# Performance work log

Hardware: AMD Instinct MI355X
Metric: run time of the kernel (lower is better)

## Reference

```python
import jax, jax.numpy as jnp
import numpy as np
import math

B = 16
IMG = 224
P = 16
C_IN = 3
E = 768
H = 12
HD = E // H          # 64
D = 6                # depth
MLP = 3072
NC = 1000
GH = IMG // P        # 14
N = GH * GH + 1      # 197 tokens incl cls
LAMBDA_INIT = 0.8
EPS = 1e-5


def setup_inputs() -> dict:
    key = jax.random.key(0)
    ks = jax.random.split(key, 24)
    s = 0.02
    inp = {
        "x": jax.random.normal(ks[0], (B, C_IN, IMG, IMG), jnp.float32),
        "conv_w": jax.random.normal(ks[1], (E, C_IN, P, P), jnp.float32) * s,
        "conv_b": jnp.zeros((E,), jnp.float32),
        "cls_token": jax.random.normal(ks[2], (1, 1, E), jnp.float32) * s,
        "pos_embed": jax.random.normal(ks[3], (1, N, E), jnp.float32) * s,
        # per-layer stacked params (leading dim D)
        "Wq": jax.random.normal(ks[4], (D, E, 2 * E), jnp.float32) * s,
        "Wk": jax.random.normal(ks[5], (D, E, 2 * E), jnp.float32) * s,
        "Wv": jax.random.normal(ks[6], (D, E, 2 * E), jnp.float32) * s,
        "lq1": jax.random.normal(ks[7], (D, H, HD), jnp.float32) * 0.1,
        "lk1": jax.random.normal(ks[8], (D, H, HD), jnp.float32) * 0.1,
        "lq2": jax.random.normal(ks[9], (D, H, HD), jnp.float32) * 0.1,
        "lk2": jax.random.normal(ks[10], (D, H, HD), jnp.float32) * 0.1,
        "gn_g": jnp.ones((D, 2 * HD), jnp.float32),
        "gn_b": jnp.zeros((D, 2 * HD), jnp.float32),
        "Wo": jax.random.normal(ks[11], (D, 2 * E, E), jnp.float32) * s,
        "ln1_g": jnp.ones((D, E), jnp.float32),
        "ln1_b": jnp.zeros((D, E), jnp.float32),
        "ln2_g": jnp.ones((D, E), jnp.float32),
        "ln2_b": jnp.zeros((D, E), jnp.float32),
        "mlp_w1": jax.random.normal(ks[12], (D, E, MLP), jnp.float32) * s,
        "mlp_b1": jnp.zeros((D, MLP), jnp.float32),
        "mlp_w2": jax.random.normal(ks[13], (D, MLP, E), jnp.float32) * s,
        "mlp_b2": jnp.zeros((D, E), jnp.float32),
        "lnf_g": jnp.ones((E,), jnp.float32),
        "lnf_b": jnp.zeros((E,), jnp.float32),
        "head_w": jax.random.normal(ks[14], (E, NC), jnp.float32) * s,
        "head_b": jnp.zeros((NC,), jnp.float32),
    }
    return inp


def _ln(z, g, b):
    m = jnp.mean(z, axis=-1, keepdims=True)
    v = jnp.var(z, axis=-1, keepdims=True)
    return (z - m) * jax.lax.rsqrt(v + EPS) * g + b


def _forward(x, conv_w, conv_b, cls_token, pos_embed, Wq, Wk, Wv,
             lq1, lk1, lq2, lk2, gn_g, gn_b, Wo,
             ln1_g, ln1_b, ln2_g, ln2_b,
             mlp_w1, mlp_b1, mlp_w2, mlp_b2,
             lnf_g, lnf_b, head_w, head_b):
    Bx = x.shape[0]
    # patch embedding (conv stride=kernel == non-overlapping patch matmul)
    xp = x.reshape(Bx, C_IN, GH, P, GH, P)
    tok = jnp.einsum('bchpwq,ecpq->bhwe', xp, conv_w).reshape(Bx, GH * GH, E) + conv_b
    h = jnp.concatenate([jnp.broadcast_to(cls_token, (Bx, 1, E)), tok], axis=1) + pos_embed

    scale = 1.0 / math.sqrt(HD)

    def block(h, p):
        xn = _ln(h, p['ln1_g'], p['ln1_b'])
        q = (xn @ p['Wq']).reshape(Bx, N, H, 2 * HD).transpose(0, 2, 1, 3)
        k = (xn @ p['Wk']).reshape(Bx, N, H, 2 * HD).transpose(0, 2, 1, 3)
        v = (xn @ p['Wv']).reshape(Bx, N, H, 2 * HD).transpose(0, 2, 1, 3)
        q1, q2 = q[..., :HD], q[..., HD:]
        k1, k2 = k[..., :HD], k[..., HD:]
        a1 = jax.nn.softmax(jnp.einsum('bhnd,bhmd->bhnm', q1, k1) * scale, axis=-1)
        a2 = jax.nn.softmax(jnp.einsum('bhnd,bhmd->bhnm', q2, k2) * scale, axis=-1)
        lam = (jnp.exp(jnp.sum(p['lq1'] * p['lk1'], axis=-1))
               - jnp.exp(jnp.sum(p['lq2'] * p['lk2'], axis=-1)) + LAMBDA_INIT)  # (H,)
        attn = a1 - lam[None, :, None, None] * a2
        o = jnp.einsum('bhnm,bhmd->bhnd', attn, v)  # (B,H,N,2HD)
        # GroupNorm(1 group) over (N, 2HD) per (b,h) sample, per-channel affine
        m = jnp.mean(o, axis=(2, 3), keepdims=True)
        var = jnp.var(o, axis=(2, 3), keepdims=True)
        o = (o - m) * jax.lax.rsqrt(var + EPS) * p['gn_g'] + p['gn_b']
        o = o.transpose(0, 2, 1, 3).reshape(Bx, N, 2 * E) @ p['Wo']
        h = h + o
        xn2 = _ln(h, p['ln2_g'], p['ln2_b'])
        ff = jax.nn.gelu(xn2 @ p['mlp_w1'] + p['mlp_b1'], approximate=False) @ p['mlp_w2'] + p['mlp_b2']
        return h + ff, attn

    params = dict(Wq=Wq, Wk=Wk, Wv=Wv, lq1=lq1, lk1=lk1, lq2=lq2, lk2=lk2,
                  gn_g=gn_g, gn_b=gn_b, Wo=Wo, ln1_g=ln1_g, ln1_b=ln1_b,
                  ln2_g=ln2_g, ln2_b=ln2_b, mlp_w1=mlp_w1, mlp_b1=mlp_b1,
                  mlp_w2=mlp_w2, mlp_b2=mlp_b2)
    h, attns = jax.lax.scan(block, h, params)
    h = _ln(h, lnf_g, lnf_b)
    logits = h[:, 0] @ head_w + head_b
    return logits, attns  # attns: (D, B, H, N, N)


def reference(x, conv_w, conv_b, cls_token, pos_embed, Wq, Wk, Wv,
              lq1, lk1, lq2, lk2, gn_g, gn_b, Wo,
              ln1_g, ln1_b, ln2_g, ln2_b,
              mlp_w1, mlp_b1, mlp_w2, mlp_b2,
              lnf_g, lnf_b, head_w, head_b):
    return _forward(x, conv_w, conv_b, cls_token, pos_embed, Wq, Wk, Wv,
                    lq1, lk1, lq2, lk2, gn_g, gn_b, Wo,
                    ln1_g, ln1_b, ln2_g, ln2_b,
                    mlp_w1, mlp_b1, mlp_w2, mlp_b2,
                    lnf_g, lnf_b, head_w, head_b)
```

## Files before the change

kernel.cpp:

```cpp
#include <hip/hip_runtime.h>
#include <hip/hip_bf16.h>
#include <math.h>

#define BB 16
#define NT 197
#define EE 768
#define HH 12
#define E2 1536
#define MLPD 3072
#define NCLS 1000
#define ND 6
#define EPSF 1e-5f
#define SCALEF 0.125f
#define LAMINIT 0.8f
#define TOKC 3152

using v8bf  = __attribute__((ext_vector_type(8))) __bf16;
using f32x4 = __attribute__((ext_vector_type(4))) float;
typedef __hip_bfloat16 bf16;

#define AS1 __attribute__((address_space(1)))
#define AS3 __attribute__((address_space(3)))

__device__ __forceinline__ void gld16(const void* g, void* l) {
    __builtin_amdgcn_global_load_lds((const AS1 void*)g, (AS3 void*)l, 16, 0, 0);
}

__device__ __forceinline__ float gelu_f(float x) {
    const float u = x + 0.044715f * x * x * x;
    const float e = __expf(fminf(1.5957691216f * u, 80.f));
    return x * e / (e + 1.f);
}

__global__ __launch_bounds__(256) void gemm_bf16(
    const bf16* __restrict__ A, const bf16* __restrict__ Wt,
    const float* __restrict__ bias, float* __restrict__ C0,
    float* __restrict__ C1, float* __restrict__ C2,
    const float* __restrict__ pos, int M, int K, int ldA, int ldB, int Nc, int mode)
{
    __shared__ __align__(16) unsigned char smem[32768];
    const int t = threadIdx.x;
    const int wave = t >> 6, lane = t & 63;
    const int wr = wave >> 1, wc = wave & 1;
    const int lr = lane & 15, lk = lane >> 4;

    const int bid0 = blockIdx.y * gridDim.x + blockIdx.x;
    const int nwg = gridDim.x * gridDim.y;
    const int qv = nwg >> 3, rv = nwg & 7;
    const int xcd = bid0 & 7, ii = bid0 >> 3;
    const int wgid = (xcd < rv ? xcd * (qv + 1) : rv * (qv + 1) + (xcd - rv) * qv) + ii;
    const int rowBase = (wgid / gridDim.x) * 128;
    const int colBase = (wgid % gridDim.x) * 128;
    const size_t zoff = (size_t)blockIdx.z * K * 2;

    f32x4 acc[4][4];
#pragma unroll
    for (int i = 0; i < 4; ++i)
#pragma unroll
        for (int j = 0; j < 4; ++j) acc[i][j] = (f32x4){0.f,0.f,0.f,0.f};

    const size_t ldA2 = (size_t)ldA * 2, ldB2 = (size_t)ldB * 2;
    const int srow = t >> 3;
    const int schunk = (t & 7) ^ ((t >> 3) & 7);
    const char* Abase = (const char*)A + zoff + schunk * 16;
    const char* Bbase = (const char*)Wt + zoff + schunk * 16;
    unsigned char* lA = smem + t * 16;
    unsigned char* lB = smem + 16384 + t * 16;
    const v8bf* Sa = (const v8bf*)smem;
    const v8bf* Sb = (const v8bf*)(smem + 16384);

    int rA[4], rB[4];
#pragma unroll
    for (int c = 0; c < 4; ++c) {
        rA[c] = min(rowBase + c * 32 + srow, M - 1);
        rB[c] = colBase + c * 32 + srow;
    }

    for (int k0 = 0; k0 < K; k0 += 64) {
        const size_t kb = (size_t)k0 * 2;
#pragma unroll
        for (int c = 0; c < 4; ++c) {
            gld16(Abase + (size_t)rA[c] * ldA2 + kb, lA + c * 4096);
            gld16(Bbase + (size_t)rB[c] * ldB2 + kb, lB + c * 4096);
        }
        __syncthreads();
#pragma unroll
        for (int s = 0; s < 2; ++s) {
            const int xr_ = (s * 4 + lk) ^ (lr & 7);
            v8bf af[4], bfr[4];
#pragma unroll
            for (int i = 0; i < 4; ++i) af[i] = Sa[(wr * 64 + i * 16 + lr) * 8 + xr_];
#pragma unroll
            for (int j = 0; j < 4; ++j) bfr[j] = Sb[(wc * 64 + j * 16 + lr) * 8 + xr_];
#pragma unroll
            for (int i = 0; i < 4; ++i)
#pragma unroll
                for (int j = 0; j < 4; ++j)
                    acc[i][j] = __builtin_amdgcn_mfma_f32_16x16x32_bf16(af[i], bfr[j], acc[i][j], 0, 0, 0);
        }
        __syncthreads();
    }

    if (mode == 0) {
        float* Cs = (float*)smem;
        float* C0z = C0 + (size_t)blockIdx.z * M * Nc;
#pragma unroll
        for (int half = 0; half < 2; ++half) {
            __syncthreads();
            if (wr == half) {
#pragma unroll
                for (int i = 0; i < 4; ++i)
#pragma unroll
                    for (int j = 0; j < 4; ++j)
#pragma unroll
                        for (int rr = 0; rr < 4; ++rr)
                            Cs[(i*16 + lk*4 + rr)*128 + wc*64 + j*16 + lr] = acc[i][j][rr];
            }
            __syncthreads();
#pragma unroll
            for (int k = 0; k < 8; ++k) {
                const int idx = k*256 + t;
                const int row = idx >> 5, c4 = idx & 31;
                const int r = rowBase + half*64 + row;
                if (r < M)
                    *(float4*)&C0z[(size_t)r*Nc + colBase + c4*4] = *(float4*)&Cs[row*128 + c4*4];
            }
        }
    } else if (mode == 1) {
        const int which = colBase / E2;
        if (which == 2) {
#pragma unroll
            for (int i = 0; i < 4; ++i)
#pragma unroll
                for (int j = 0; j < 4; ++j)
#pragma unroll
                    for (int rr = 0; rr < 4; ++rr) {
                        const int r = rowBase + wr * 64 + i * 16 + lk * 4 + rr;
                        const int c = colBase + wc * 64 + j * 16 + lr;
                        if (r >= M) continue;
                        const int b_ = r / NT, n_ = r % NT;
                        const int cc = c % E2;
                        const int h_ = cc >> 7, d_ = cc & 127;
                        const size_t bh = (size_t)(b_ * HH + h_);
                        ((bf16*)C2)[((bh * 7 + (n_ >> 5)) * 8 + (d_ >> 4)) * 512 +
                                    (size_t)(((d_ & 15) + (((n_ >> 3) & 3) << 4)) * 8 + (n_ & 7))] =
                            __float2bfloat16(acc[i][j][rr]);
                    }
        } else {
            const int hFix = (colBase % E2) >> 7;
            bf16* dstBase = (bf16*)(which == 0 ? C0 : C1);
            bf16* Cs = (bf16*)smem;
            __syncthreads();
#pragma unroll
            for (int i = 0; i < 4; ++i)
#pragma unroll
                for (int j = 0; j < 4; ++j)
#pragma unroll
                    for (int rr = 0; rr < 4; ++rr)
                        Cs[(wr*64 + i*16 + lk*4 + rr)*128 + wc*64 + j*16 + lr] =
                            __float2bfloat16(acc[i][j][rr]);
            __syncthreads();
#pragma unroll
            for (int k = 0; k < 8; ++k) {
                const int idx = k*256 + t;
                const int row = idx >> 4, c8 = idx & 15;
                const int r = rowBase + row;
                if (r < M) {
                    const int b_ = r / NT, n_ = r - b_ * NT;
                    const size_t bh = (size_t)(b_ * HH + hFix);
                    *(uint4*)(dstBase + (bh * 208 + n_) * 128 + c8 * 8) =
                        *(uint4*)&Cs[row*128 + c8*8];
                }
            }
        }
    } else if (mode == 3) {
        bf16* Cs = (bf16*)smem;
        __syncthreads();
#pragma unroll
        for (int i = 0; i < 4; ++i)
#pragma unroll
            for (int j = 0; j < 4; ++j)
#pragma unroll
                for (int rr = 0; rr < 4; ++rr) {
                    const int c = colBase + wc*64 + j*16 + lr;
                    float val = acc[i][j][rr] + bias[c];
                    Cs[(wr*64 + i*16 + lk*4 + rr)*128 + wc*64 + j*16 + lr] =
                        __float2bfloat16(gelu_f(val));
                }
        __syncthreads();
        bf16* C0b = (bf16*)C0;
#pragma unroll
        for (int k = 0; k < 8; ++k) {
            const int idx = k*256 + t;
            const int row = idx >> 4, c8 = idx & 15;
            const int r = rowBase + row;
            if (r < M)
                *(uint4*)(C0b + (size_t)r*Nc + colBase + c8*8) = *(uint4*)&Cs[row*128 + c8*8];
        }
    } else {
#pragma unroll
        for (int i = 0; i < 4; ++i)
#pragma unroll
            for (int j = 0; j < 4; ++j)
#pragma unroll
                for (int rr = 0; rr < 4; ++rr) {
                    const int r = rowBase + wr * 64 + i * 16 + lk * 4 + rr;
                    const int c = colBase + wc * 64 + j * 16 + lr;
                    if (r >= M) continue;
                    const int b_ = r / 196, p_ = r % 196;
                    C0[((size_t)(b_ * NT) + 1 + p_) * EE + c] =
                        acc[i][j][rr] + bias[c] + pos[(size_t)(1 + p_) * EE + c];
                }
    }
}

__global__ __launch_bounds__(512, 2) void gemm256(
    const bf16* __restrict__ A, const bf16* __restrict__ Wt,
    const float* __restrict__ bias, float* __restrict__ C0,
    float* __restrict__ C1, float* __restrict__ C2,
    int M, int K, int Nc, int mode)
{
    __shared__ __align__(16) unsigned char smem[131072];
    const int t = threadIdx.x;
    const int wave = t >> 6, lane = t & 63;
    const int wm = wave >> 2, wn = wave & 3;
    const int lr = lane & 15, lk = lane >> 4;

    const int bid0 = blockIdx.y * gridDim.x + blockIdx.x;
    const int nwg = gridDim.x * gridDim.y;
    const int qv = nwg >> 3, rv = nwg & 7;
    const int xcd = bid0 & 7, ii = bid0 >> 3;
    const int wgid = (xcd < rv ? xcd * (qv + 1) : rv * (qv + 1) + (xcd - rv) * qv) + ii;
    const int rowBase = (wgid / gridDim.x) * 256;
    const int colBase = (wgid % gridDim.x) * 256;

    f32x4 acc[8][4];
#pragma unroll
    for (int i = 0; i < 8; ++i)
#pragma unroll
        for (int j = 0; j < 4; ++j) acc[i][j] = (f32x4){0.f,0.f,0.f,0.f};

    const size_t ldK2 = (size_t)K * 2;
    const int srow = t >> 3;
    const int schunk = (t & 7) ^ (srow & 7);
    const char* Abase = (const char*)A + schunk * 16;
    const char* Bbase = (const char*)Wt + schunk * 16;

    int rA[4], rB[4];
#pragma unroll
    for (int p = 0; p < 4; ++p) {
        rA[p] = min(rowBase + p * 64 + srow, M - 1);
        rB[p] = colBase + p * 64 + srow;
    }

    {
        unsigned char* l0 = smem + t * 16;
#pragma unroll
        for (int p = 0; p < 4; ++p) {
            gld16(Abase + (size_t)rA[p] * ldK2, l0 + p * 8192);
            gld16(Bbase + (size_t)rB[p] * ldK2, l0 + 32768 + p * 8192);
        }
#pragma unroll
        for (int p = 0; p < 4; ++p) {
            gld16(Abase + (size_t)rA[p] * ldK2 + 128, l0 + 65536 + p * 8192);
            gld16(Bbase + (size_t)rB[p] * ldK2 + 128, l0 + 65536 + 32768 + p * 8192);
        }
        asm volatile("s_waitcnt vmcnt(8)" ::: "memory");
        asm volatile("s_barrier" ::: "memory");
    }

    const int NTt = K >> 6;
    for (int kt = 0; kt < NTt; ++kt) {
        const int buf = kt & 1;
        const v8bf* Sa = (const v8bf*)(smem + buf * 65536);
        const v8bf* Sb = (const v8bf*)(smem + buf * 65536 + 32768);

        v8bf bfr[2][4], af[2][4];
#pragma unroll
        for (int s = 0; s < 2; ++s) {
            const int x0 = s * 4 + lk;
#pragma unroll
            for (int j = 0; j < 4; ++j) {
                const int row = wn * 64 + j * 16 + lr;
                bfr[s][j] = Sb[row * 8 + (x0 ^ (lr & 7))];
            }
#pragma unroll
            for (int i = 0; i < 4; ++i) {
                const int row = wm * 128 + i * 16 + lr;
                af[s][i] = Sa[row * 8 + (x0 ^ (lr & 7))];
            }
        }
        __builtin_amdgcn_s_setprio(1);
#pragma unroll
        for (int s = 0; s < 2; ++s)
#pragma unroll
            for (int i = 0; i < 4; ++i)
#pragma unroll
                for (int j = 0; j < 4; ++j)
                    acc[i][j] = __builtin_amdgcn_mfma_f32_16x16x32_bf16(af[s][i], bfr[s][j], acc[i][j], 0, 0, 0);
        __builtin_amdgcn_s_setprio(0);

        v8bf af2[2][4];
#pragma unroll
        for (int s = 0; s < 2; ++s)
#pragma unroll
            for (int i = 0; i < 4; ++i) {
                const int row = wm * 128 + 64 + i * 16 + lr;
                af2[s][i] = Sa[row * 8 + ((s * 4 + lk) ^ (lr & 7))];
            }
        asm volatile("s_waitcnt lgkmcnt(0)" ::: "memory");
        asm volatile("s_barrier" ::: "memory");
        if (kt + 2 < NTt) {
            const size_t kb = (size_t)(kt + 2) * 128;
            unsigned char* ld = smem + buf * 65536 + t * 16;
#pragma unroll
            for (int p = 0; p < 4; ++p) {
                gld16(Abase + (size_t)rA[p] * ldK2 + kb, ld + p * 8192);
                gld16(Bbase + (size_t)rB[p] * ldK2 + kb, ld + 32768 + p * 8192);
            }
            asm volatile("s_waitcnt vmcnt(8)" ::: "memory");
        } else {
            asm volatile("s_waitcnt vmcnt(0)" ::: "memory");
        }
        asm volatile("s_barrier" ::: "memory");
        __builtin_amdgcn_s_setprio(1);
#pragma unroll
        for (int s = 0; s < 2; ++s)
#pragma unroll
            for (int i = 0; i < 4; ++i)
#pragma unroll
                for (int j = 0; j < 4; ++j)
                    acc[4 + i][j] = __builtin_amdgcn_mfma_f32_16x16x32_bf16(af2[s][i], bfr[s][j], acc[4 + i][j], 0, 0, 0);
        __builtin_amdgcn_s_setprio(0);
    }

    if (mode == 1) {
        const int which = colBase / E2;
        if (which == 2) {
#pragma unroll
            for (int i = 0; i < 8; ++i)
#pragma unroll
                for (int j = 0; j < 4; ++j)
#pragma unroll
                    for (int rr = 0; rr < 4; ++rr) {
                        const int r = rowBase + wm * 128 + i * 16 + lk * 4 + rr;
                        if (r >= M) continue;
                        const int c = colBase + wn * 64 + j * 16 + lr;
                        const int b_ = r / NT, n_ = r % NT;
                        const int cc = c % E2;
                        const int h_ = cc >> 7, d_ = cc & 127;
                        const size_t bh = (size_t)(b_ * HH + h_);
                        ((bf16*)C2)[((bh * 7 + (n_ >> 5)) * 8 + (d_ >> 4)) * 512 +
                                    (size_t)(((d_ & 15) + (((n_ >> 3) & 3) << 4)) * 8 + (n_ & 7))] =
                            __float2bfloat16(acc[i][j][rr]);
                    }
        } else {
            bf16* dstBase = (bf16*)(which == 0 ? C0 : C1);
            const int h0 = (colBase % E2) >> 7;
            bf16* Cs = (bf16*)smem;
            __syncthreads();
#pragma unroll
            for (int i = 0; i < 8; ++i)
#pragma unroll
                for (int j = 0; j < 4; ++j)
#pragma unroll
                    for (int rr = 0; rr < 4; ++rr)
                        Cs[(wm*128 + i*16 + lk*4 + rr)*256 + wn*64 + j*16 + lr] =
                            __float2bfloat16(acc[i][j][rr]);
            __syncthreads();
#pragma unroll
            for (int k = 0; k < 16; ++k) {
                const int idx = k * 512 + t;
                const int row = idx >> 5, c8 = idx & 31;
                const int r = rowBase + row;
                if (r < M) {
                    const int b_ = r / NT, n_ = r - b_ * NT;
                    const size_t bh = (size_t)(b_ * HH + h0 + (c8 >> 4));
                    *(uint4*)(dstBase + (bh * 208 + n_) * 128 + (size_t)(c8 & 15) * 8) =
                        *(uint4*)&Cs[row * 256 + c8 * 8];
                }
            }
        }
    } else {
        bf16* Cs = (bf16*)smem;
        __syncthreads();
#pragma unroll
        for (int i = 0; i < 8; ++i)
#pragma unroll
            for (int j = 0; j < 4; ++j) {
                const int c = colBase + wn * 64 + j * 16 + lr;
                const float bv = bias[c];
#pragma unroll
                for (int rr = 0; rr < 4; ++rr)
                    Cs[(wm*128 + i*16 + lk*4 + rr)*256 + wn*64 + j*16 + lr] =
                        __float2bfloat16(gelu_f(acc[i][j][rr] + bv));
            }
        __syncthreads();
        bf16* C0b = (bf16*)C0;
#pragma unroll
        for (int k = 0; k < 16; ++k) {
            const int idx = k * 512 + t;
            const int row = idx >> 5, c8 = idx & 31;
            const int r = rowBase + row;
            if (r < M)
                *(uint4*)(C0b + (size_t)r * Nc + colBase + c8 * 8) =
                    *(uint4*)&Cs[row * 256 + c8 * 8];
        }
    }
}

__global__ __launch_bounds__(64) void attn_mfma(
    const bf16* __restrict__ Qrm, const bf16* __restrict__ Krm,
    const bf16* __restrict__ Vf, const float* __restrict__ lamp,
    float* __restrict__ aout, float* __restrict__ o, float* __restrict__ stats)
{
    const int lane = threadIdx.x;
    const int fid = blockIdx.x;
    const int xcd = fid & 7, rest = fid >> 3;
    const int qt = rest % 13, g = rest / 13;
    const int bh = g * 8 + xcd;
    const int hh = bh % HH;
    const int lr = lane & 15, lk = lane >> 4;

    __shared__ __align__(16) bf16 P[16][232];

    {
        const int r = lane & 15, c0 = 192 + (lane >> 4) * 10;
#pragma unroll
        for (int j = 0; j < 10; ++j) P[r][c0 + j] = __float2bfloat16(0.f);
    }

    v8bf qa[4];
    const bf16* Qb = Qrm + ((size_t)bh * 208 + qt * 16) * 128;
#pragma unroll
    for (int kk = 0; kk < 4; ++kk)
        qa[kk] = *(const v8bf*)(Qb + lr * 128 + kk * 32 + lk * 8);

    const bf16* Kb = Krm + (size_t)bh * 208 * 128;
    const f32x4 zf = {0.f, 0.f, 0.f, 0.f};
    f32x4 s1[13], s2[13];
#pragma unroll
    for (int t = 0; t < 13; ++t) {
        const bf16* Kt = Kb + (t * 16 + lr) * 128 + lk * 8;
        const v8bf k0 = *(const v8bf*)(Kt);
        const v8bf k1 = *(const v8bf*)(Kt + 32);
        const v8bf k2 = *(const v8bf*)(Kt + 64);
        const v8bf k3 = *(const v8bf*)(Kt + 96);
        s1[t] = __builtin_amdgcn_mfma_f32_16x16x32_bf16(qa[1], k1,
                __builtin_amdgcn_mfma_f32_16x16x32_bf16(qa[0], k0, zf, 0, 0, 0), 0, 0, 0);
        s2[t] = __builtin_amdgcn_mfma_f32_16x16x32_bf16(qa[3], k3,
                __builtin_amdgcn_mfma_f32_16x16x32_bf16(qa[2], k2, zf, 0, 0, 0), 0, 0, 0);
    }

    float m1[4] = {-1e30f,-1e30f,-1e30f,-1e30f}, m2[4] = {-1e30f,-1e30f,-1e30f,-1e30f};
#pragma unroll
    for (int t = 0; t < 13; ++t) {
        const bool kv = (t * 16 + lr) < NT;
#pragma unroll
        for (int rr = 0; rr < 4; ++rr) {
            s1[t][rr] = kv ? s1[t][rr] * SCALEF : -1e30f;
            s2[t][rr] = kv ? s2[t][rr] * SCALEF : -1e30f;
            m1[rr] = fmaxf(m1[rr], s1[t][rr]);
            m2[rr] = fmaxf(m2[rr], s2[t][rr]);
        }
    }
#pragma unroll
    for (int off = 8; off >= 1; off >>= 1)
#pragma unroll
        for (int rr = 0; rr < 4; ++rr) {
            m1[rr] = fmaxf(m1[rr], __shfl_xor(m1[rr], off));
            m2[rr] = fmaxf(m2[rr], __shfl_xor(m2[rr], off));
        }

    float z1[4] = {0,0,0,0}, z2[4] = {0,0,0,0};
#pragma unroll
    for (int t = 0; t < 13; ++t)
#pragma unroll
        for (int rr = 0; rr < 4; ++rr) {
            const float e1 = __expf(s1[t][rr] - m1[rr]);
            const float e2 = __expf(s2[t][rr] - m2[rr]);
            s1[t][rr] = e1; s2[t][rr] = e2;
            z1[rr] += e1; z2[rr] += e2;
        }
#pragma unroll
    for (int off = 8; off >= 1; off >>= 1)
#pragma unroll
        for (int rr = 0; rr < 4; ++rr) {
            z1[rr] += __shfl_xor(z1[rr], off);
            z2[rr] += __shfl_xor(z2[rr], off);
        }
    const float lam = lamp[hh];
    float r1[4], r2[4];
#pragma unroll
    for (int rr = 0; rr < 4; ++rr) { r1[rr] = 1.f / z1[rr]; r2[rr] = lam / z2[rr]; }

    __syncthreads();
#pragma unroll
    for (int t = 0; t < 13; ++t) {
        const int m_ = t * 16 + lr;
#pragma unroll
        for (int rr = 0; rr < 4; ++rr) {
            const float p = s1[t][rr] * r1[rr] - s2[t][rr] * r2[rr];
            const int n_ = lk * 4 + rr;
            P[n_][m_] = __float2bfloat16(p);
            const int n_g = qt * 16 + n_;
            if (m_ < NT && n_g < NT)
                aout[((size_t)bh * NT + n_g) * NT + m_] = p;
        }
    }
    __syncthreads();

    f32x4 oacc[8];
#pragma unroll
    for (int dt = 0; dt < 8; ++dt) oacc[dt] = zf;
    const v8bf* Vp = (const v8bf*)(Vf + (size_t)bh * 7 * 8 * 512);
    const bf16* Pb = &P[0][0];
#pragma unroll
    for (int mk = 0; mk < 7; ++mk) {
        const v8bf pa = *(const v8bf*)(Pb + lr * 232 + mk * 32 + lk * 8);
#pragma unroll
        for (int dt = 0; dt < 8; ++dt)
            oacc[dt] = __builtin_amdgcn_mfma_f32_16x16x32_bf16(
                pa, Vp[(mk * 8 + dt) * 64 + lane], oacc[dt], 0, 0, 0);
    }
#pragma unroll
    for (int dt = 0; dt < 8; ++dt)
#pragma unroll
        for (int rr = 0; rr < 4; ++rr) {
            const int n_g = qt * 16 + lk * 4 + rr;
            if (n_g < NT)
                o[((size_t)bh * NT + n_g) * 128 + dt * 16 + lr] = oacc[dt][rr];
        }

    float s = 0.f, ss = 0.f;
#pragma unroll
    for (int dt = 0; dt < 8; ++dt)
#pragma unroll
        for (int rr = 0; rr < 4; ++rr) {
            const int n_g = qt * 16 + lk * 4 + rr;
            const float vv = (n_g < NT) ? oacc[dt][rr] : 0.f;
            s += vv; ss += vv * vv;
        }
#pragma unroll
    for (int off = 32; off >= 1; off >>= 1) {
        s  += __shfl_xor(s, off);
        ss += __shfl_xor(ss, off);
    }
    if (lane == 0) {
        stats[(bh * 13 + qt) * 2]     = s;
        stats[(bh * 13 + qt) * 2 + 1] = ss;
    }
}

__global__ __launch_bounds__(256) void gn_apply(
    const float* __restrict__ o, const float* __restrict__ stats,
    const float* __restrict__ g, const float* __restrict__ bb, bf16* __restrict__ o2)
{
    const int bh = blockIdx.y, qq = blockIdx.x;
    const int t = threadIdx.x;
    float S = 0.f, SS = 0.f;
#pragma unroll
    for (int j = 0; j < 13; ++j) {
        S  += stats[(bh * 13 + j) * 2];
        SS += stats[(bh * 13 + j) * 2 + 1];
    }
    const float inv = 1.f / (float)(NT * 128);
    const float mean = S * inv;
    const float var  = SS * inv - mean * mean;
    const float rstd = rsqrtf(var + EPSF);
    const int b_ = bh / HH, h_ = bh % HH;
    const float4* ob = (const float4*)(o + (size_t)bh * NT * 128);
    const float4* g4 = (const float4*)g;
    const float4* b4 = (const float4*)bb;
    for (int idx = t; idx < 50 * 32; idx += 256) {
        const int n_ = qq * 50 + (idx >> 5);
        if (n_ >= NT) continue;
        const int d4 = idx & 31;
        const float4 v4 = ob[n_ * 32 + d4];
        const float4 gg = g4[d4], bv = b4[d4];
        bf16 tmp[4];
        tmp[0] = __float2bfloat16((v4.x - mean) * rstd * gg.x + bv.x);
        tmp[1] = __float2bfloat16((v4.y - mean) * rstd * gg.y + bv.y);
        tmp[2] = __float2bfloat16((v4.z - mean) * rstd * gg.z + bv.z);
        tmp[3] = __float2bfloat16((v4.w - mean) * rstd * gg.w + bv.w);
        *(uint2*)(o2 + ((size_t)(b_ * NT + n_)) * E2 + h_ * 128 + d4 * 4) = *(uint2*)tmp;
    }
}

__global__ __launch_bounds__(256) void ln_rows(
    const float* __restrict__ in, const float* __restrict__ g,
    const float* __restrict__ bb, bf16* __restrict__ out)
{
    const int r = blockIdx.x;
    const int t = threadIdx.x;
    const float* x = in + (size_t)r * EE;
    const float v0 = x[t], v1 = x[t+256], v2 = x[t+512];
    __shared__ float rs[256], rss[256];
    rs[t]  = v0+v1+v2;
    rss[t] = v0*v0+v1*v1+v2*v2;
    __syncthreads();
    for (int st = 128; st > 0; st >>= 1) {
        if (t < st) { rs[t] += rs[t+st]; rss[t] += rss[t+st]; }
        __syncthreads();
    }
    const float mean = rs[0] * (1.f/768.f);
    const float var  = rss[0] * (1.f/768.f) - mean*mean;
    const float rstd = rsqrtf(var + EPSF);
    bf16* o = out + (size_t)r * EE;
    o[t]     = __float2bfloat16((v0-mean)*rstd*g[t]     + bb[t]);
    o[t+256] = __float2bfloat16((v1-mean)*rstd*g[t+256] + bb[t+256]);
    o[t+512] = __float2bfloat16((v2-mean)*rstd*g[t+512] + bb[t+512]);
}

__global__ __launch_bounds__(192) void ln_fuse(
    const float* __restrict__ hin, const float* __restrict__ Pp,
    const float* __restrict__ bias, const float* __restrict__ g,
    const float* __restrict__ bb, float* __restrict__ hout, bf16* __restrict__ xout)
{
    const int r = blockIdx.x;
    const int t = threadIdx.x;
    const int lane = t & 63, wv = t >> 6;
    const size_t base4 = (size_t)r * 192 + t;
    float4 v = ((const float4*)hin)[base4];
    const float4 p0 = ((const float4*)Pp)[base4];
    const float4 p1 = ((const float4*)Pp)[(size_t)TOKC * 192 + base4];
    v.x += p0.x + p1.x; v.y += p0.y + p1.y; v.z += p0.z + p1.z; v.w += p0.w + p1.w;
    if (bias) {
        const float4 bv = ((const float4*)bias)[t];
        v.x += bv.x; v.y += bv.y; v.z += bv.z; v.w += bv.w;
    }
    float s  = v.x + v.y + v.z + v.w;
    float ss = v.x*v.x + v.y*v.y + v.z*v.z + v.w*v.w;
#pragma unroll
    for (int off = 32; off >= 1; off >>= 1) {
        s  += __shfl_xor(s, off);
        ss += __shfl_xor(ss, off);
    }
    __shared__ float ws_[3][2];
    if (lane == 0) { ws_[wv][0] = s; ws_[wv][1] = ss; }
    __syncthreads();
    const float S  = ws_[0][0] + ws_[1][0] + ws_[2][0];
    const float SS = ws_[0][1] + ws_[1][1] + ws_[2][1];
    const float mean = S * (1.f/768.f);
    const float var  = SS * (1.f/768.f) - mean*mean;
    const float rstd = rsqrtf(var + EPSF);
    ((float4*)hout)[base4] = v;
    const float4 gg = ((const float4*)g)[t];
    const float4 bv2 = ((const float4*)bb)[t];
    bf16 tmp[4];
    tmp[0] = __float2bfloat16((v.x-mean)*rstd*gg.x + bv2.x);
    tmp[1] = __float2bfloat16((v.y-mean)*rstd*gg.y + bv2.y);
    tmp[2] = __float2bfloat16((v.z-mean)*rstd*gg.z + bv2.z);
    tmp[3] = __float2bfloat16((v.w-mean)*rstd*gg.w + bv2.w);
    *(uint2*)(xout + base4 * 4) = *(uint2*)tmp;
}

__global__ void lam_kernel(const float* __restrict__ lq1, const float* __restrict__ lk1,
                           const float* __restrict__ lq2, const float* __restrict__ lk2,
                           float* __restrict__ lam)
{
    const int i = threadIdx.x;
    if (i < ND*HH) {
        float d1 = 0.f, d2 = 0.f;
        for (int d = 0; d < 64; ++d) {
            d1 += lq1[i*64+d]*lk1[i*64+d];
            d2 += lq2[i*64+d]*lk2[i*64+d];
        }
        lam[i] = expf(d1) - expf(d2) + LAMINIT;
    }
}

__global__ void cls_kernel(const float* __restrict__ cls, const float* __restrict__ pos,
                           float* __restrict__ h)
{
    const int i = blockIdx.x*256 + threadIdx.x;
    if (i < BB*EE) {
        const int b_ = i / EE, e_ = i % EE;
        h[(size_t)(b_*NT)*EE + e_] = cls[e_] + pos[e_];
    }
}

__global__ void im2col_kernel(const float* __restrict__ x, bf16* __restrict__ xcol)
{
    const int i = blockIdx.x*256 + threadIdx.x;
    if (i >= 3136*EE) return;
    const int kidx = i % EE;
    const int p_ = i / EE;
    const int b_ = p_ / 196;
    const int pp = p_ % 196;
    const int gh = pp / 14, gw = pp % 14;
    const int c_ = kidx >> 8, rr = (kidx >> 4) & 15, q_ = kidx & 15;
    xcol[i] = __float2bfloat16(x[((size_t)(b_*3 + c_)*224 + gh*16 + rr)*224 + gw*16 + q_]);
}

__global__ void convert_flat(const float* __restrict__ in, bf16* __restrict__ out, int n)
{
    const int i = blockIdx.x*256 + threadIdx.x;
    if (i < n) out[i] = __float2bfloat16(in[i]);
}

__global__ void transpose_pack(const float* __restrict__ Wq, const float* __restrict__ Wk,
                               const float* __restrict__ Wv, const float* __restrict__ Wo,
                               const float* __restrict__ W1, const float* __restrict__ W2,
                               bf16* __restrict__ wall)
{
    __shared__ float tile[64][65];
    int bid = blockIdx.x;
    const int dl = bid / 2304; bid -= dl * 2304;
    bf16* wq_t = wall + (size_t)dl * 9437184;
    bf16* wo_t = wq_t + 3538944;
    bf16* w1_t = wo_t + 1179648;
    bf16* w2_t = w1_t + 2359296;
    const float* src; bf16* dst; int K, N, gx;
    if (bid < 864) {
        const int z = bid / 288; bid -= z * 288;
        src = (z == 0 ? Wq : (z == 1 ? Wk : Wv)) + (size_t)dl * EE * E2;
        dst = wq_t + (size_t)z * E2 * EE; K = EE; N = E2; gx = 24;
    } else if (bid < 1152) { src = Wo + (size_t)dl*E2*EE; dst = wo_t; K = E2; N = EE; gx = 12; bid -= 864; }
    else if (bid < 1728)   { src = W1 + (size_t)dl*EE*MLPD; dst = w1_t; K = EE; N = MLPD; gx = 48; bid -= 1152; }
    else                   { src = W2 + (size_t)dl*MLPD*EE; dst = w2_t; K = MLPD; N = EE; gx = 12; bid -= 1728; }
    const int bx = bid % gx, by = bid / gx;
    const int t = threadIdx.x;
    const int n0 = bx*64, k0 = by*64;
    {
        const int c4 = t & 15, kr = t >> 4;
#pragma unroll
        for (int i = 0; i < 4; ++i) {
            const int row = i * 16 + kr;
            const float4 v = *(const float4*)(src + (size_t)(k0 + row) * N + n0 + c4 * 4);
            tile[row][c4*4+0] = v.x; tile[row][c4*4+1] = v.y;
            tile[row][c4*4+2] = v.z; tile[row][c4*4+3] = v.w;
        }
    }
    __syncthreads();
    {
        const int ko = t & 7, nb = t >> 3;
#pragma unroll
        for (int i = 0; i < 2; ++i) {
            const int n = i * 32 + nb;
            bf16 tmp[8];
#pragma unroll
            for (int j = 0; j < 8; ++j)
                tmp[j] = __float2bfloat16(tile[ko*8+j][n]);
            *(uint4*)(dst + (size_t)(n0 + n) * K + k0 + ko * 8) = *(uint4*)tmp;
        }
    }
}

__global__ __launch_bounds__(256) void ln_cls(
    const float* __restrict__ h, const float* __restrict__ g,
    const float* __restrict__ bb, float* __restrict__ xr)
{
    const int b_ = blockIdx.x;
    const int t = threadIdx.x;
    const float* x = h + (size_t)(b_*NT)*EE;
    const float v0 = x[t], v1 = x[t+256], v2 = x[t+512];
    __shared__ float rs[256], rss[256];
    rs[t]  = v0+v1+v2;
    rss[t] = v0*v0+v1*v1+v2*v2;
    __syncthreads();
    for (int st = 128; st > 0; st >>= 1) {
        if (t < st) { rs[t] += rs[t+st]; rss[t] += rss[t+st]; }
        __syncthreads();
    }
    const float mean = rs[0] * (1.f/768.f);
    const float var  = rss[0] * (1.f/768.f) - mean*mean;
    const float rstd = rsqrtf(var + EPSF);
    float* o = xr + (size_t)b_ * EE;
    o[t]     = (v0-mean)*rstd*g[t]     + bb[t];
    o[t+256] = (v1-mean)*rstd*g[t+256] + bb[t+256];
    o[t+512] = (v2-mean)*rstd*g[t+512] + bb[t+512];
}

__global__ __launch_bounds__(256) void head_gemm(
    const float* __restrict__ xr, const float* __restrict__ hw,
    const float* __restrict__ hb, float* __restrict__ logits)
{
    const int b_ = blockIdx.y, ct = blockIdx.x;
    const int t = threadIdx.x;
    const int c_loc = t & 63, kp = t >> 6;
    const int c = ct * 64 + c_loc;
    __shared__ float xs[768];
    for (int i = t; i < 768; i += 256) xs[i] = xr[(size_t)b_*EE + i];
    __syncthreads();
    float acc = 0.f;
    if (c < NCLS) {
        const int k0 = kp * 192;
        for (int kk = k0; kk < k0 + 192; ++kk)
            acc += xs[kk] * hw[(size_t)kk * NCLS + c];
    }
    __shared__ float red[4][64];
    red[kp][c_loc] = acc;
    __syncthreads();
    if (kp == 0 && c < NCLS)
        logits[(size_t)b_*NCLS + c] =
            red[0][c_loc] + red[1][c_loc] + red[2][c_loc] + red[3][c_loc] + hb[c];
}

extern "C" void kernel_launch(void* const* d_in, const int* in_sizes, int n_in,
                              void* d_out, int out_size, void* d_ws, size_t ws_size,
                              hipStream_t stream)
{
    const float* x      = (const float*)d_in[0];
    const float* conv_w = (const float*)d_in[1];
    const float* conv_b = (const float*)d_in[2];
    const float* cls    = (const float*)d_in[3];
    const float* pos    = (const float*)d_in[4];
    const float* Wq     = (const float*)d_in[5];
    const float* Wk     = (const float*)d_in[6];
    const float* Wv     = (const float*)d_in[7];
    const float* lq1    = (const float*)d_in[8];
    const float* lk1    = (const float*)d_in[9];
    const float* lq2    = (const float*)d_in[10];
    const float* lk2    = (const float*)d_in[11];
    const float* gn_g   = (const float*)d_in[12];
    const float* gn_b   = (const float*)d_in[13];
    const float* Wo     = (const float*)d_in[14];
    const float* ln1_g  = (const float*)d_in[15];
    const float* ln1_b  = (const float*)d_in[16];
    const float* ln2_g  = (const float*)d_in[17];
    const float* ln2_b  = (const float*)d_in[18];
    const float* mlp_w1 = (const float*)d_in[19];
    const float* mlp_b1 = (const float*)d_in[20];
    const float* mlp_w2 = (const float*)d_in[21];
    const float* mlp_b2 = (const float*)d_in[22];
    const float* lnf_g  = (const float*)d_in[23];
    const float* lnf_b  = (const float*)d_in[24];
    const float* head_w = (const float*)d_in[25];
    const float* head_b = (const float*)d_in[26];

    float* out_f    = (float*)d_out;
    float* logits   = out_f;
    float* attn_out = out_f + (size_t)BB*NCLS;

    const int TOK = TOKC;
    const size_t TOKE = (size_t)TOK*EE;

    float* ws   = (float*)d_ws;
    float* h    = ws;
    float* o    = h + TOKE;
    float* Pp   = o + (size_t)BB*HH*NT*128;
    bf16*  Qrm  = (bf16*)(Pp + 2*TOKE);
    bf16*  Krm  = Qrm + (size_t)192*208*128;
    bf16*  Vf   = Krm + (size_t)192*208*128;
    bf16*  act2 = Vf + (size_t)192*7*8*512;
    bf16*  xn   = act2 + (size_t)TOK*MLPD;
    bf16*  wall = xn + TOKE;
    bf16*  cwbf = wall + (size_t)6*9437184;
    float* lam  = (float*)(cwbf + (size_t)EE*EE);
    float* xr   = lam + 128;
    float* gnst = xr + (size_t)BB*EE;

    hipMemsetAsync(Vf, 0, (size_t)192*7*8*512*2, stream);

    lam_kernel<<<1, 128, 0, stream>>>(lq1, lk1, lq2, lk2, lam);
    convert_flat<<<(EE*EE+255)/256, 256, 0, stream>>>(conv_w, cwbf, EE*EE);
    transpose_pack<<<6*2304, 256, 0, stream>>>(Wq, Wk, Wv, Wo, mlp_w1, mlp_w2, wall);
    im2col_kernel<<<(3136*EE+255)/256, 256, 0, stream>>>(x, xn);
    cls_kernel<<<(BB*EE+255)/256, 256, 0, stream>>>(cls, pos, h);
    gemm_bf16<<<dim3(EE/128, 25), 256, 0, stream>>>(
        xn, cwbf, conv_b, h, nullptr, nullptr, pos, 3136, EE, EE, EE, EE, 4);

    ln_rows<<<TOK, 256, 0, stream>>>(h, ln1_g, ln1_b, xn);

    for (int dl = 0; dl < ND; ++dl) {
        bf16* wq_t = wall + (size_t)dl*9437184;
        bf16* wo_t = wq_t + 3538944;
        bf16* w1_t = wo_t + 1179648;
        bf16* w2_t = w1_t + 2359296;

        gemm256<<<dim3(4608/256, (TOK+255)/256), 512, 0, stream>>>(
            xn, wq_t, nullptr, (float*)Qrm, (float*)Krm, (float*)Vf,
            TOK, EE, 4608, 1);
        attn_mfma<<<2496, 64, 0, stream>>>(
            Qrm, Krm, Vf, lam + dl*HH, attn_out + (size_t)dl*BB*HH*NT*NT, o, gnst);
        gn_apply<<<dim3(4, BB*HH), 256, 0, stream>>>(
            o, gnst, gn_g + dl*128, gn_b + dl*128, act2);
        gemm_bf16<<<dim3(EE/128, 25, 2), 256, 0, stream>>>(
            act2, wo_t, nullptr, Pp, nullptr, nullptr, nullptr,
            TOK, E2/2, E2, E2, EE, 0);
        ln_fuse<<<TOK, 192, 0, stream>>>(
            h, Pp, nullptr, ln2_g + dl*EE, ln2_b + dl*EE, h, xn);
        gemm256<<<dim3(MLPD/256, (TOK+255)/256), 512, 0, stream>>>(
            xn, w1_t, mlp_b1 + dl*MLPD, (float*)act2, nullptr, nullptr,
            TOK, EE, MLPD, 3);
        gemm_bf16<<<dim3(EE/128, 25, 2), 256, 0, stream>>>(
            act2, w2_t, nullptr, Pp, nullptr, nullptr, nullptr,
            TOK, MLPD/2, MLPD, MLPD, EE, 0);
        if (dl < ND-1)
            ln_fuse<<<TOK, 192, 0, stream>>>(
                h, Pp, mlp_b2 + dl*EE, ln1_g + (dl+1)*EE, ln1_b + (dl+1)*EE, h, xn);
        else
            ln_fuse<<<TOK, 192, 0, stream>>>(
                h, Pp, mlp_b2 + dl*EE, lnf_g, lnf_b, h, xn);
    }

    ln_cls<<<BB, 256, 0, stream>>>(h, lnf_g, lnf_b, xr);
    head_gemm<<<dim3(16, BB), 256, 0, stream>>>(xr, head_w, head_b, logits);
}
```

Baseline: 1.437 ms.

## Template gemm256 on N-tile width, use 192-wide tiles for MLP up-proj

Makes the 256-row GEMM kernel a template on the number of 64-column B sub-tiles and launches the MLP first-layer GEMM with 192-wide column tiles, giving 16x13 blocks instead of 12x13 so the grid fills the CUs better. It also merges the lambda, conv-weight conversion and cls-token kernels into one launch. The weight transpose-pack kernel now handles four 64-row k-tiles per block with a double-buffered shared tile and register prefetch. The narrower tile lowers per-block arithmetic intensity and changes the vmcnt wait counts.

```diff
diff --git a/kernel.cpp b/kernel.cpp
--- a/kernel.cpp
+++ b/kernel.cpp
@@ -214,13 +214,16 @@
     }
 }
 
-__global__ __launch_bounds__(512, 2) void gemm256(
+template<int NF>
+__global__ __launch_bounds__(512, 2) void gemm256t(
     const bf16* __restrict__ A, const bf16* __restrict__ Wt,
     const float* __restrict__ bias, float* __restrict__ C0,
     float* __restrict__ C1, float* __restrict__ C2,
     int M, int K, int Nc, int mode)
 {
-    __shared__ __align__(16) unsigned char smem[131072];
+    constexpr int NB = NF * 64;
+    constexpr int BUFSZ = 32768 + NF * 8192;
+    __shared__ __align__(16) unsigned char smem[2 * BUFSZ];
     const int t = threadIdx.x;
     const int wave = t >> 6, lane = t & 63;
     const int wm = wave >> 2, wn = wave & 3;
@@ -232,13 +235,13 @@
     const int xcd = bid0 & 7, ii = bid0 >> 3;
     const int wgid = (xcd < rv ? xcd * (qv + 1) : rv * (qv + 1) + (xcd - rv) * qv) + ii;
     const int rowBase = (wgid / gridDim.x) * 256;
-    const int colBase = (wgid % gridDim.x) * 256;
-
-    f32x4 acc[8][4];
+    const int colBase = (wgid % gridDim.x) * NB;
+
+    f32x4 acc[8][NF];
 #pragma unroll
     for (int i = 0; i < 8; ++i)
 #pragma unroll
-        for (int j = 0; j < 4; ++j) acc[i][j] = (f32x4){0.f,0.f,0.f,0.f};
+        for (int j = 0; j < NF; ++j) acc[i][j] = (f32x4){0.f,0.f,0.f,0.f};
 
     const size_t ldK2 = (size_t)K * 2;
     const int srow = t >> 3;
@@ -246,42 +249,40 @@
     const char* Abase = (const char*)A + schunk * 16;
     const char* Bbase = (const char*)Wt + schunk * 16;
 
-    int rA[4], rB[4];
-#pragma unroll
-    for (int p = 0; p < 4; ++p) {
-        rA[p] = min(rowBase + p * 64 + srow, M - 1);
-        rB[p] = colBase + p * 64 + srow;
-    }
+    int rA[4], rB[NF];
+#pragma unroll
+    for (int p = 0; p < 4; ++p) rA[p] = min(rowBase + p * 64 + srow, M - 1);
+#pragma unroll
+    for (int p = 0; p < NF; ++p) rB[p] = colBase + p * 64 + srow;
 
     {
         unsigned char* l0 = smem + t * 16;
 #pragma unroll
-        for (int p = 0; p < 4; ++p) {
-            gld16(Abase + (size_t)rA[p] * ldK2, l0 + p * 8192);
-            gld16(Bbase + (size_t)rB[p] * ldK2, l0 + 32768 + p * 8192);
-        }
-#pragma unroll
-        for (int p = 0; p < 4; ++p) {
-            gld16(Abase + (size_t)rA[p] * ldK2 + 128, l0 + 65536 + p * 8192);
-            gld16(Bbase + (size_t)rB[p] * ldK2 + 128, l0 + 65536 + 32768 + p * 8192);
-        }
-        asm volatile("s_waitcnt vmcnt(8)" ::: "memory");
+        for (int p = 0; p < 4; ++p) gld16(Abase + (size_t)rA[p] * ldK2, l0 + p * 8192);
+#pragma unroll
+        for (int p = 0; p < NF; ++p) gld16(Bbase + (size_t)rB[p] * ldK2, l0 + 32768 + p * 8192);
+#pragma unroll
+        for (int p = 0; p < 4; ++p) gld16(Abase + (size_t)rA[p] * ldK2 + 128, l0 + BUFSZ + p * 8192);
+#pragma unroll
+        for (int p = 0; p < NF; ++p) gld16(Bbase + (size_t)rB[p] * ldK2 + 128, l0 + BUFSZ + 32768 + p * 8192);
+        if constexpr (NF == 4) asm volatile("s_waitcnt vmcnt(8)" ::: "memory");
+        else                   asm volatile("s_waitcnt vmcnt(7)" ::: "memory");
         asm volatile("s_barrier" ::: "memory");
     }
 
     const int NTt = K >> 6;
     for (int kt = 0; kt < NTt; ++kt) {
         const int buf = kt & 1;
-        const v8bf* Sa = (const v8bf*)(smem + buf * 65536);
-        const v8bf* Sb = (const v8bf*)(smem + buf * 65536 + 32768);
-
-        v8bf bfr[2][4], af[2][4];
+        const v8bf* Sa = (const v8bf*)(smem + buf * BUFSZ);
+        const v8bf* Sb = (const v8bf*)(smem + buf * BUFSZ + 32768);
+
+        v8bf bfr[2][NF], af[2][4];
 #pragma unroll
         for (int s = 0; s < 2; ++s) {
             const int x0 = s * 4 + lk;
 #pragma unroll
-            for (int j = 0; j < 4; ++j) {
-                const int row = wn * 64 + j * 16 + lr;
+            for (int j = 0; j < NF; ++j) {
+                const int row = wn * (NF * 16) + j * 16 + lr;
                 bfr[s][j] = Sb[row * 8 + (x0 ^ (lr & 7))];
             }
 #pragma unroll
@@ -296,7 +297,7 @@
 #pragma unroll
             for (int i = 0; i < 4; ++i)
 #pragma unroll
-                for (int j = 0; j < 4; ++j)
+                for (int j = 0; j < NF; ++j)
                     acc[i][j] = __builtin_amdgcn_mfma_f32_16x16x32_bf16(af[s][i], bfr[s][j], acc[i][j], 0, 0, 0);
         __builtin_amdgcn_s_setprio(0);
 
@@ -312,13 +313,13 @@
         asm volatile("s_barrier" ::: "memory");
         if (kt + 2 < NTt) {
             const size_t kb = (size_t)(kt + 2) * 128;
-            unsigned char* ld = smem + buf * 65536 + t * 16;
-#pragma unroll
-            for (int p = 0; p < 4; ++p) {
-                gld16(Abase + (size_t)rA[p] * ldK2 + kb, ld + p * 8192);
-                gld16(Bbase + (size_t)rB[p] * ldK2 + kb, ld + 32768 + p * 8192);
-            }
-            asm volatile("s_waitcnt vmcnt(8)" ::: "memory");
+            unsigned char* ld = smem + buf * BUFSZ + t * 16;
+#pragma unroll
+            for (int p = 0; p < 4; ++p) gld16(Abase + (size_t)rA[p] * ldK2 + kb, ld + p * 8192);
+#pragma unroll
+            for (int p = 0; p < NF; ++p) gld16(Bbase + (size_t)rB[p] * ldK2 + kb, ld + 32768 + p * 8192);
+            if constexpr (NF == 4) asm volatile("s_waitcnt vmcnt(8)" ::: "memory");
+            else                   asm volatile("s_waitcnt vmcnt(7)" ::: "memory");
         } else {
             asm volatile("s_waitcnt vmcnt(0)" ::: "memory");
         }
@@ -329,82 +330,88 @@
 #pragma unroll
             for (int i = 0; i < 4; ++i)
 #pragma unroll
-                for (int j = 0; j < 4; ++j)
+                for (int j = 0; j < NF; ++j)
                     acc[4 + i][j] = __builtin_amdgcn_mfma_f32_16x16x32_bf16(af2[s][i], bfr[s][j], acc[4 + i][j], 0, 0, 0);
         __builtin_amdgcn_s_setprio(0);
     }
 
-    if (mode == 1) {
-        const int which = colBase / E2;
-        if (which == 2) {
-#pragma unroll
-            for (int i = 0; i < 8; ++i)
-#pragma unroll
-                for (int j = 0; j < 4; ++j)
-#pragma unroll
-                    for (int rr = 0; rr < 4; ++rr) {
-                        const int r = rowBase + wm * 128 + i * 16 + lk * 4 + rr;
-                        if (r >= M) continue;
-                        const int c = colBase + wn * 64 + j * 16 + lr;
-                        const int b_ = r / NT, n_ = r % NT;
-                        const int cc = c % E2;
-                        const int h_ = cc >> 7, d_ = cc & 127;
-                        const size_t bh = (size_t)(b_ * HH + h_);
-                        ((bf16*)C2)[((bh * 7 + (n_ >> 5)) * 8 + (d_ >> 4)) * 512 +
-                                    (size_t)(((d_ & 15) + (((n_ >> 3) & 3) << 4)) * 8 + (n_ & 7))] =
-                            __float2bfloat16(acc[i][j][rr]);
+    if constexpr (NF == 4) {
+        if (mode == 1) {
+            const int which = colBase / E2;
+            if (which == 2) {
+#pragma unroll
+                for (int i = 0; i < 8; ++i)
+#pragma unroll
+                    for (int j = 0; j < 4; ++j)
+#pragma unroll
+                        for (int rr = 0; rr < 4; ++rr) {
+                            const int r = rowBase + wm * 128 + i * 16 + lk * 4 + rr;
+                            if (r >= M) continue;
+                            const int c = colBase + wn * 64 + j * 16 + lr;
+                            const int b_ = r / NT, n_ = r % NT;
+                            const int cc = c % E2;
+                            const int h_ = cc >> 7, d_ = cc & 127;
+                            const size_t bh = (size_t)(b_ * HH + h_);
+                            ((bf16*)C2)[((bh * 7 + (n_ >> 5)) * 8 + (d_ >> 4)) * 512 +
+                                        (size_t)(((d_ & 15) + (((n_ >> 3) & 3) << 4)) * 8 + (n_ & 7))] =
+                                __float2bfloat16(acc[i][j][rr]);
+                        }
+            } else {
+                bf16* dstBase = (bf16*)(which == 0 ? C0 : C1);
+                const int h0 = (colBase % E2) >> 7;
+                bf16* Cs = (bf16*)smem;
+                __syncthreads();
+#pragma unroll
+                for (int i = 0; i < 8; ++i)
+#pragma unroll
+                    for (int j = 0; j < 4; ++j)
+#pragma unroll
+                        for (int rr = 0; rr < 4; ++rr)
+                            Cs[(wm*128 + i*16 + lk*4 + rr)*256 + wn*64 + j*16 + lr] =
+                                __float2bfloat16(acc[i][j][rr]);
+                __syncthreads();
+#pragma unroll
+                for (int k = 0; k < 16; ++k) {
+                    const int idx = k * 512 + t;
+                    const int row = idx >> 5, c8 = idx & 31;
+                    const int r = rowBase + row;
+                    if (r < M) {
+                        const int b_ = r / NT, n_ = r - b_ * NT;
+                        const size_t bh = (size_t)(b_ * HH + h0 + (c8 >> 4));
+                        *(uint4*)(dstBase + (bh * 208 + n_) * 128 + (size_t)(c8 & 15) * 8) =
+                            *(uint4*)&Cs[row * 256 + c8 * 8];
                     }
-        } else {
-            bf16* dstBase = (bf16*)(which == 0 ? C0 : C1);
-            const int h0 = (colBase % E2) >> 7;
-            bf16* Cs = (bf16*)smem;
-            __syncthreads();
-#pragma unroll
-            for (int i = 0; i < 8; ++i)
-#pragma unroll
-                for (int j = 0; j < 4; ++j)
-#pragma unroll
-                    for (int rr = 0; rr < 4; ++rr)
-                        Cs[(wm*128 + i*16 + lk*4 + rr)*256 + wn*64 + j*16 + lr] =
-                            __float2bfloat16(acc[i][j][rr]);
-            __syncthreads();
-#pragma unroll
-            for (int k = 0; k < 16; ++k) {
-                const int idx = k * 512 + t;
-                const int row = idx >> 5, c8 = idx & 31;
-                const int r = rowBase + row;
-                if (r < M) {
-                    const int b_ = r / NT, n_ = r - b_ * NT;
-                    const size_t bh = (size_t)(b_ * HH + h0 + (c8 >> 4));
-                    *(uint4*)(dstBase + (bh * 208 + n_) * 128 + (size_t)(c8 & 15) * 8) =
-                        *(uint4*)&Cs[row * 256 + c8 * 8];
                 }
             }
-        }
-    } else {
+            return;
+        }
+    }
+    {
         bf16* Cs = (bf16*)smem;
         __syncthreads();
 #pragma unroll
         for (int i = 0; i < 8; ++i)
 #pragma unroll
-            for (int j = 0; j < 4; ++j) {
-                const int c = colBase + wn * 64 + j * 16 + lr;
+            for (int j = 0; j < NF; ++j) {
+                const int c = colBase + wn * (NF * 16) + j * 16 + lr;
                 const float bv = bias[c];
 #pragma unroll
                 for (int rr = 0; rr < 4; ++rr)
-                    Cs[(wm*128 + i*16 + lk*4 + rr)*256 + wn*64 + j*16 + lr] =
+                    Cs[(wm*128 + i*16 + lk*4 + rr)*NB + wn*(NF*16) + j*16 + lr] =
                         __float2bfloat16(gelu_f(acc[i][j][rr] + bv));
             }
         __syncthreads();
         bf16* C0b = (bf16*)C0;
-#pragma unroll
-        for (int k = 0; k < 16; ++k) {
+        constexpr int CW = NB / 8;
+        constexpr int ITER = 256 * CW / 512;
+#pragma unroll
+        for (int k = 0; k < ITER; ++k) {
             const int idx = k * 512 + t;
-            const int row = idx >> 5, c8 = idx & 31;
+            const int row = idx / CW, c8 = idx - row * CW;
             const int r = rowBase + row;
             if (r < M)
                 *(uint4*)(C0b + (size_t)r * Nc + colBase + c8 * 8) =
-                    *(uint4*)&Cs[row * 256 + c8 * 8];
+                    *(uint4*)&Cs[row * NB + c8 * 8];
         }
     }
 }
@@ -655,28 +662,31 @@
     *(uint2*)(xout + base4 * 4) = *(uint2*)tmp;
 }
 
-__global__ void lam_kernel(const float* __restrict__ lq1, const float* __restrict__ lk1,
+__global__ void setup_misc(const float* __restrict__ conv_w, bf16* __restrict__ cwbf,
+                           const float* __restrict__ cls, const float* __restrict__ pos,
+                           float* __restrict__ h,
+                           const float* __restrict__ lq1, const float* __restrict__ lk1,
                            const float* __restrict__ lq2, const float* __restrict__ lk2,
                            float* __restrict__ lam)
 {
-    const int i = threadIdx.x;
-    if (i < ND*HH) {
-        float d1 = 0.f, d2 = 0.f;
-        for (int d = 0; d < 64; ++d) {
-            d1 += lq1[i*64+d]*lk1[i*64+d];
-            d2 += lq2[i*64+d]*lk2[i*64+d];
-        }
-        lam[i] = expf(d1) - expf(d2) + LAMINIT;
-    }
-}
-
-__global__ void cls_kernel(const float* __restrict__ cls, const float* __restrict__ pos,
-                           float* __restrict__ h)
-{
-    const int i = blockIdx.x*256 + threadIdx.x;
-    if (i < BB*EE) {
+    const int bid = blockIdx.x;
+    if (bid < 2304) {
+        const int i = bid * 256 + threadIdx.x;
+        cwbf[i] = __float2bfloat16(conv_w[i]);
+    } else if (bid < 2352) {
+        const int i = (bid - 2304) * 256 + threadIdx.x;
         const int b_ = i / EE, e_ = i % EE;
         h[(size_t)(b_*NT)*EE + e_] = cls[e_] + pos[e_];
+    } else {
+        const int i = threadIdx.x;
+        if (i < ND*HH) {
+            float d1 = 0.f, d2 = 0.f;
+            for (int d = 0; d < 64; ++d) {
+                d1 += lq1[i*64+d]*lk1[i*64+d];
+                d2 += lq2[i*64+d]*lk2[i*64+d];
+            }
+            lam[i] = expf(d1) - expf(d2) + LAMINIT;
+        }
     }
 }
 
@@ -693,56 +703,62 @@
     xcol[i] = __float2bfloat16(x[((size_t)(b_*3 + c_)*224 + gh*16 + rr)*224 + gw*16 + q_]);
 }
 
-__global__ void convert_flat(const float* __restrict__ in, bf16* __restrict__ out, int n)
-{
-    const int i = blockIdx.x*256 + threadIdx.x;
-    if (i < n) out[i] = __float2bfloat16(in[i]);
-}
-
-__global__ void transpose_pack(const float* __restrict__ Wq, const float* __restrict__ Wk,
-                               const float* __restrict__ Wv, const float* __restrict__ Wo,
-                               const float* __restrict__ W1, const float* __restrict__ W2,
-                               bf16* __restrict__ wall)
-{
-    __shared__ float tile[64][65];
+__global__ __launch_bounds__(256) void transpose_pack(
+    const float* __restrict__ Wq, const float* __restrict__ Wk,
+    const float* __restrict__ Wv, const float* __restrict__ Wo,
+    const float* __restrict__ W1, const float* __restrict__ W2,
+    bf16* __restrict__ wall)
+{
+    __shared__ float tile[2][64][65];
     int bid = blockIdx.x;
-    const int dl = bid / 2304; bid -= dl * 2304;
+    const int dl = bid / 576; bid -= dl * 576;
     bf16* wq_t = wall + (size_t)dl * 9437184;
     bf16* wo_t = wq_t + 3538944;
     bf16* w1_t = wo_t + 1179648;
     bf16* w2_t = w1_t + 2359296;
     const float* src; bf16* dst; int K, N, gx;
-    if (bid < 864) {
-        const int z = bid / 288; bid -= z * 288;
+    if (bid < 216) {
+        const int z = bid / 72; bid -= z * 72;
         src = (z == 0 ? Wq : (z == 1 ? Wk : Wv)) + (size_t)dl * EE * E2;
         dst = wq_t + (size_t)z * E2 * EE; K = EE; N = E2; gx = 24;
-    } else if (bid < 1152) { src = Wo + (size_t)dl*E2*EE; dst = wo_t; K = E2; N = EE; gx = 12; bid -= 864; }
-    else if (bid < 1728)   { src = W1 + (size_t)dl*EE*MLPD; dst = w1_t; K = EE; N = MLPD; gx = 48; bid -= 1152; }
-    else                   { src = W2 + (size_t)dl*MLPD*EE; dst = w2_t; K = MLPD; N = EE; gx = 12; bid -= 1728; }
+    } else if (bid < 288) { src = Wo + (size_t)dl*E2*EE;  dst = wo_t; K = E2;   N = EE;   gx = 12; bid -= 216; }
+    else if (bid < 432)   { src = W1 + (size_t)dl*EE*MLPD; dst = w1_t; K = EE;  N = MLPD; gx = 48; bid -= 288; }
+    else                  { src = W2 + (size_t)dl*MLPD*EE; dst = w2_t; K = MLPD; N = EE;  gx = 12; bid -= 432; }
     const int bx = bid % gx, by = bid / gx;
+    const int n0 = bx * 64, kbase = by * 256;
     const int t = threadIdx.x;
-    const int n0 = bx*64, k0 = by*64;
-    {
-        const int c4 = t & 15, kr = t >> 4;
+    const int c4 = t & 15, kr = t >> 4;
+    const int ko = t & 7, nb = t >> 3;
+
+    float4 ld[4];
+#pragma unroll
+    for (int i = 0; i < 4; ++i)
+        ld[i] = *(const float4*)(src + (size_t)(kbase + i*16 + kr) * N + n0 + c4*4);
+
+    for (int kt = 0; kt < 4; ++kt) {
+        float (*tb)[65] = tile[kt & 1];
 #pragma unroll
         for (int i = 0; i < 4; ++i) {
-            const int row = i * 16 + kr;
-            const float4 v = *(const float4*)(src + (size_t)(k0 + row) * N + n0 + c4 * 4);
-            tile[row][c4*4+0] = v.x; tile[row][c4*4+1] = v.y;
-            tile[row][c4*4+2] = v.z; tile[row][c4*4+3] = v.w;
-        }
-    }
-    __syncthreads();
-    {
-        const int ko = t & 7, nb = t >> 3;
+            const int row = i*16 + kr;
+            tb[row][c4*4+0] = ld[i].x; tb[row][c4*4+1] = ld[i].y;
+            tb[row][c4*4+2] = ld[i].z; tb[row][c4*4+3] = ld[i].w;
+        }
+        if (kt < 3) {
+            const int k0n = kbase + (kt+1)*64;
+#pragma unroll
+            for (int i = 0; i < 4; ++i)
+                ld[i] = *(const float4*)(src + (size_t)(k0n + i*16 + kr) * N + n0 + c4*4);
+        }
+        __syncthreads();
+        const int k0 = kbase + kt*64;
 #pragma unroll
         for (int i = 0; i < 2; ++i) {
-            const int n = i * 32 + nb;
+            const int n = i*32 + nb;
             bf16 tmp[8];
 #pragma unroll
             for (int j = 0; j < 8; ++j)
-                tmp[j] = __float2bfloat16(tile[ko*8+j][n]);
-            *(uint4*)(dst + (size_t)(n0 + n) * K + k0 + ko * 8) = *(uint4*)tmp;
+                tmp[j] = __float2bfloat16(tb[ko*8+j][n]);
+            *(uint4*)(dst + (size_t)(n0 + n) * K + k0 + ko*8) = *(uint4*)tmp;
         }
     }
 }
@@ -853,11 +869,10 @@
 
     hipMemsetAsync(Vf, 0, (size_t)192*7*8*512*2, stream);
 
-    lam_kernel<<<1, 128, 0, stream>>>(lq1, lk1, lq2, lk2, lam);
-    convert_flat<<<(EE*EE+255)/256, 256, 0, stream>>>(conv_w, cwbf, EE*EE);
-    transpose_pack<<<6*2304, 256, 0, stream>>>(Wq, Wk, Wv, Wo, mlp_w1, mlp_w2, wall);
+    setup_misc<<<2353, 256, 0, stream>>>(conv_w, cwbf, cls, pos, h,
+                                         lq1, lk1, lq2, lk2, lam);
+    transpose_pack<<<6*576, 256, 0, stream>>>(Wq, Wk, Wv, Wo, mlp_w1, mlp_w2, wall);
     im2col_kernel<<<(3136*EE+255)/256, 256, 0, stream>>>(x, xn);
-    cls_kernel<<<(BB*EE+255)/256, 256, 0, stream>>>(cls, pos, h);
     gemm_bf16<<<dim3(EE/128, 25), 256, 0, stream>>>(
         xn, cwbf, conv_b, h, nullptr, nullptr, pos, 3136, EE, EE, EE, EE, 4);
 
@@ -869,7 +884,7 @@
         bf16* w1_t = wo_t + 1179648;
         bf16* w2_t = w1_t + 2359296;
 
-        gemm256<<<dim3(4608/256, (TOK+255)/256), 512, 0, stream>>>(
+        gemm256t<4><<<dim3(4608/256, (TOK+255)/256), 512, 0, stream>>>(
             xn, wq_t, nullptr, (float*)Qrm, (float*)Krm, (float*)Vf,
             TOK, EE, 4608, 1);
         attn_mfma<<<2496, 64, 0, stream>>>(
@@ -881,7 +896,7 @@
             TOK, E2/2, E2, E2, EE, 0);
         ln_fuse<<<TOK, 192, 0, stream>>>(
             h, Pp, nullptr, ln2_g + dl*EE, ln2_b + dl*EE, h, xn);
-        gemm256<<<dim3(MLPD/256, (TOK+255)/256), 512, 0, stream>>>(
+        gemm256t<3><<<dim3(MLPD/192, (TOK+255)/256), 512, 0, stream>>>(
             xn, w1_t, mlp_b1 + dl*MLPD, (float*)act2, nullptr, nullptr,
             TOK, EE, MLPD, 3);
         gemm_bf16<<<dim3(EE/128, 25, 2), 256, 0, stream>>>(
```

Result: faster. 1.383 ms (-3.7%).
